# Kernel optimization log

Hardware: AMD Instinct MI355X
Metric: run time of the kernel (lower is better)

Reference implementation:

```python
import jax, jax.numpy as jnp
import numpy as np

B, N, NFEAT = 8, 5000, 15
NUM_CLASSES_IN = 12          # len(elem_labels)
D_IN = NUM_CLASSES_IN + NFEAT - 1  # 26
D_DIST = 256
D_HID = 256
BIN_SIZE = 100
NBINS = N // BIN_SIZE        # 50
K = 16                       # num_neighbors
DIST_MULT = 0.1
MAX_HALF_BINS = 100          # max_num_bins // 2
NUM_ID_OUT, NUM_REG_OUT = 8, 4


def _pairwise_dist(A):
    # A: [nbins, bs, d] -> [nbins, bs, bs]
    na = jnp.sum(A * A, -1)
    d2 = na[..., :, None] - 2.0 * jnp.einsum('...nd,...md->...nm', A, A) + na[..., None, :]
    return jnp.sqrt(jnp.maximum(d2, 1e-6))


def _build_edges(points, rot):
    # points: [N, D_DIST]; LSH binning then per-bin kNN (exp(-dist_mult * dist) affinities)
    mul = points @ rot[:, :NBINS // 2]
    cmul = jnp.concatenate([mul, -mul], axis=-1)
    bin_idx = jnp.argmax(cmul, axis=-1)
    bins_split = jnp.argsort(bin_idx).reshape(NBINS, BIN_SIZE)   # [nbins, bs] point ids
    parts = points[bins_split]                                   # [nbins, bs, d]
    dm = jnp.exp(-DIST_MULT * _pairwise_dist(parts))             # [nbins, bs, bs]
    vals, idx = jax.lax.top_k(dm, K)                             # [nbins, bs, K]
    dst = jax.vmap(lambda b, i: b[i])(bins_split, idx)           # global dst ids
    src = jnp.broadcast_to(bins_split[:, :, None], dst.shape)
    return src.reshape(-1), dst.reshape(-1), vals.reshape(-1)    # nnz = N*K


def _ghconv(x, src, dst, vals, theta, W_h, W_t, b_t):
    # x: [N, H]; edge list (src, dst, vals); duplicates sum, matching tf.sparse.add
    deg = jax.ops.segment_sum(vals, src, num_segments=N)
    norm = jnp.power(deg + 1e-6, -0.5)[:, None]
    f_hom = (x @ theta) * norm
    agg = jax.ops.segment_sum(vals[:, None] * f_hom[dst], src, num_segments=N) * norm
    f_het = x @ W_h
    gate = jax.nn.sigmoid(x @ W_t + b_t)
    return jax.nn.selu(gate * agg + (1.0 - gate) * f_het)


def setup_inputs() -> dict:
    key = jax.random.key(0)
    ks = jax.random.split(key, 32)
    w = lambda i, shape, s=0.02: (s * jax.random.normal(ks[i], shape)).astype(jnp.float32)
    ids = jax.random.randint(ks[0], (B, N, 1), 0, NUM_CLASSES_IN).astype(jnp.float32)
    props = jax.random.normal(ks[1], (B, N, NFEAT - 1), dtype=jnp.float32)
    X = jnp.concatenate([ids, props], axis=-1)
    return {
        'X': X,
        'rot': w(2, (D_DIST, MAX_HALF_BINS), 1.0),
        'W_emb': w(3, (D_IN, D_DIST)), 'b_emb': w(4, (D_DIST,)),
        'Wenc_id': w(5, (D_IN, D_HID)), 'benc_id': w(6, (D_HID,)),
        'theta_id': w(7, (D_HID, D_HID)), 'Wh_id': w(8, (D_HID, D_HID)),
        'Wt_id': w(9, (D_HID, D_HID)), 'bt_id': w(10, (D_HID,)),
        'Wdec_id': w(11, (D_HID, D_HID)), 'bdec_id': w(12, (D_HID,)),
        'Wout_id': w(13, (D_HID, NUM_ID_OUT)), 'bout_id': w(14, (NUM_ID_OUT,)),
        'Wenc_reg': w(15, (D_IN, D_HID)), 'benc_reg': w(16, (D_HID,)),
        'theta_reg': w(17, (D_HID, D_HID)), 'Wh_reg': w(18, (D_HID, D_HID)),
        'Wt_reg': w(19, (D_HID, D_HID)), 'bt_reg': w(20, (D_HID,)),
        'Wdec_reg': w(21, (D_HID, D_HID)), 'bdec_reg': w(22, (D_HID,)),
        'Wout_reg': w(23, (D_HID, NUM_REG_OUT)), 'bout_reg': w(24, (NUM_REG_OUT,)),
    }


def reference(X, rot, W_emb, b_emb,
              Wenc_id, benc_id, theta_id, Wh_id, Wt_id, bt_id, Wdec_id, bdec_id, Wout_id, bout_id,
              Wenc_reg, benc_reg, theta_reg, Wh_reg, Wt_reg, bt_reg, Wdec_reg, bdec_reg, Wout_reg, bout_reg):
    # InputEncoding: one-hot class id + remaining features
    enc = jnp.concatenate(
        [jax.nn.one_hot(X[:, :, 0].astype(jnp.int32), NUM_CLASSES_IN, dtype=jnp.float32),
         X[:, :, 1:]], axis=-1)                                  # [B, N, 26]
    emb = enc @ W_emb + b_emb                                     # distance embedding
    src, dst, vals = jax.vmap(_build_edges, in_axes=(0, None))(emb, rot)

    def branch(Wenc, benc, theta, Wh, Wt, bt, Wdec, bdec, Wout, bout):
        x = jax.nn.selu(enc @ Wenc + benc)
        x = jax.vmap(lambda xb, s, d, v: _ghconv(xb, s, d, v, theta, Wh, Wt, bt))(x, src, dst, vals)
        x = jax.nn.selu(x @ Wdec + bdec)
        return x @ Wout + bout

    out_id = branch(Wenc_id, benc_id, theta_id, Wh_id, Wt_id, bt_id, Wdec_id, bdec_id, Wout_id, bout_id)
    out_reg = branch(Wenc_reg, benc_reg, theta_reg, Wh_reg, Wt_reg, bt_reg, Wdec_reg, bdec_reg, Wout_reg, bout_reg)
    return out_id, out_reg
```

## Files before the change

### kernel.cpp

```cpp
#include <hip/hip_runtime.h>
#include <hip/hip_bf16.h>
#include <cstdint>
#include <cstddef>

#define NB     8
#define NLOC   5000
#define NPTS   40000
#define DIN    26
#define DH     256
#define NBINS  50
#define BSZ    100
#define KNN    16
#define KP     104

static const size_t OFF_BHI  = 40960000;
static const size_t OFF_BLO  = 41353216;
static const size_t OFF_BDHI = 41746432;
static const size_t OFF_BDLO = 41877504;
static const size_t OFF_ENC  = 81920000;
static const size_t OFF_BIN  = 86080000;
static const size_t OFF_ORD  = 86240000;
static const size_t OFF_NRM  = 86400000;
static const size_t OFF_EVAL = 86560000;
static const size_t OFF_EDST = 89120000;
static const size_t OFF_KEYS = 91680000;
static const size_t OFF_AXHI = 91680000;
static const size_t OFF_AXLO = 112160000;
static const size_t OFF_NA   = 132640000;
static const size_t OFF_FHET = 132640000;
static const size_t OFF_GATE = 173600000;

typedef __attribute__((ext_vector_type(8))) short short8;
typedef __attribute__((ext_vector_type(4))) float f32x4;

__device__ __forceinline__ float selu_f(float x) {
  const float scale = 1.0507009873554805f, alpha = 1.6732632423543772f;
  return x > 0.f ? scale * x : scale * alpha * expm1f(x);
}

__device__ __forceinline__ void split_bf16(float v, __hip_bfloat16& h, __hip_bfloat16& l) {
  h = __float2bfloat16(v);
  l = __float2bfloat16(v - __bfloat162float(h));
}

#define EPB 16
__global__ __launch_bounds__(256) void k_enc_emb(
    const float* __restrict__ X, const float* __restrict__ Wemb,
    const float* __restrict__ bemb, float* __restrict__ enc,
    double* __restrict__ emb) {
  __shared__ float xb[EPB * 15];
  const int tid = threadIdx.x;
  const int r0 = blockIdx.x * EPB;
  if (tid < EPB * 15) xb[tid] = X[(size_t)r0 * 15 + tid];
  double wcol[DIN];
  #pragma unroll
  for (int c = 0; c < DIN; c++) wcol[c] = (double)Wemb[c * DH + tid];
  const double bcol = (double)bemb[tid];
  __syncthreads();
  #pragma unroll 1
  for (int p = 0; p < EPB; p++) {
    const int id = (int)xb[p * 15];
    double acc = 0.0;
    #pragma unroll
    for (int c = 0; c < 12; c++)
      acc += ((c == id) ? 1.0 : 0.0) * wcol[c];
    #pragma unroll
    for (int c = 12; c < DIN; c++)
      acc += (double)xb[p * 15 + (c - 11)] * wcol[c];
    emb[(size_t)(r0 + p) * DH + tid] = acc + bcol;
  }
  #pragma unroll
  for (int t = 0; t < 2; t++) {
    int idx = t * 256 + tid;
    if (idx < EPB * DIN) {
      int p = idx / DIN, c = idx - p * DIN;
      int id = (int)xb[p * 15];
      float v = (c < 12) ? ((c == id) ? 1.f : 0.f) : xb[p * 15 + (c - 11)];
      enc[(size_t)(r0 + p) * DIN + c] = v;
    }
  }
}

#define MULPTS 16
__global__ __launch_bounds__(512) void k_mul(
    const double* __restrict__ emb, const float* __restrict__ rot,
    int* __restrict__ bin_idx) {
  __shared__ double ebuf[MULPTS][258];
  __shared__ float  rotT[25][257];
  __shared__ double mulb[MULPTS][26];
  const int tid = threadIdx.x;
  const int r0 = blockIdx.x * MULPTS;
  for (int idx = tid; idx < 25 * DH; idx += 512) {
    int d = idx / 25, j = idx - d * 25;
    rotT[j][d] = rot[d * 100 + j];
  }
  for (int idx = tid; idx < MULPTS * DH; idx += 512) {
    int p = idx >> 8, d = idx & 255;
    ebuf[p][d] = emb[(size_t)(r0 + p) * DH + d];
  }
  __syncthreads();
  if (tid < MULPTS * 25) {
    int p = tid / 25, j = tid - p * 25;
    double a = 0.0;
    #pragma unroll 4
    for (int d = 0; d < DH; d++) a += ebuf[p][d] * (double)rotT[j][d];
    mulb[p][j] = a;
  }
  __syncthreads();
  if (tid < MULPTS) {
    double best = -1e300; int bi = 0;
    #pragma unroll 1
    for (int jj = 0; jj < 2 * 25; jj++) {
      double v = (jj < 25) ? mulb[tid][jj] : -mulb[tid][jj - 25];
      if (v > best) { best = v; bi = jj; }
    }
    bin_idx[r0 + tid] = bi;
  }
}

#define SCH 20
__global__ __launch_bounds__(256) void k_sort(
    const int* __restrict__ bin_idx, int* __restrict__ order) {
  const int b = blockIdx.x;
  __shared__ unsigned short cnt[256][NBINS + 2];
  __shared__ int base[NBINS];
  __shared__ int bl[NLOC];
  const int tid = threadIdx.x;
  for (int j = 0; j < NBINS; j++) cnt[tid][j] = 0;
  for (int n = tid; n < NLOC; n += 256) bl[n] = bin_idx[b * NLOC + n];
  __syncthreads();
  const int s = tid * SCH;
  const int e = (s + SCH < NLOC) ? s + SCH : NLOC;
  for (int n = s; n < e; n++) cnt[tid][bl[n]]++;
  __syncthreads();
  if (tid < NBINS) {
    int run = 0;
    for (int t = 0; t < 256; t++) {
      int c = cnt[t][tid];
      cnt[t][tid] = (unsigned short)run;
      run += c;
    }
    base[tid] = run;
  }
  __syncthreads();
  if (tid == 0) {
    int r = 0;
    for (int j = 0; j < NBINS; j++) { int t = base[j]; base[j] = r; r += t; }
  }
  __syncthreads();
  for (int n = s; n < e; n++) {
    int j = bl[n];
    int pos = base[j] + cnt[tid][j];
    cnt[tid][j]++;
    order[b * NLOC + pos] = n;
  }
}

__global__ __launch_bounds__(256) void k_norm(
    const double* __restrict__ emb, const int* __restrict__ order,
    double* __restrict__ na) {
  const int s = blockIdx.x * 4 + (threadIdx.x >> 6);
  const int lane = threadIdx.x & 63;
  const int row = (s / NLOC) * NLOC + order[s];
  const double* p = &emb[(size_t)row * DH + lane * 4];
  double2 a = *(const double2*)p;
  double2 b = *(const double2*)(p + 2);
  double sum = a.x * a.x + a.y * a.y + b.x * b.x + b.y * b.y;
  #pragma unroll
  for (int off = 32; off >= 1; off >>= 1) sum += __shfl_xor(sum, off);
  if (lane == 0) na[s] = sum;
}

#define DQR 112
__global__ __launch_bounds__(256) void k_dist(
    const double* __restrict__ emb, const int* __restrict__ order,
    const double* __restrict__ na, double* __restrict__ keys) {
  __shared__ double P[DQR][34];
  __shared__ double naL[DQR];
  __shared__ int rid[DQR];
  const int bin = blockIdx.x;
  const int rh  = blockIdx.y;
  const int gb0 = bin * BSZ;
  const int brow = (bin / NBINS) * NLOC;
  const int tid = threadIdx.x;
  const int tx = tid & 15, ty = tid >> 4;
  if (tid < DQR) {
    int rr = tid < BSZ ? tid : BSZ - 1;
    rid[tid] = brow + order[gb0 + rr];
    naL[tid] = na[gb0 + rr];
  }
  __syncthreads();
  size_t srow[7];
  int scol[7], sr[7];
  #pragma unroll
  for (int q = 0; q < 7; q++) {
    int idx = q * 256 + tid;
    sr[q] = idx >> 4;
    scol[q] = (idx & 15) * 2;
    srow[q] = (size_t)rid[sr[q]] * DH;
  }
  int ar[4];
  #pragma unroll
  for (int i = 0; i < 4; i++) {
    int pr = rh * 50 + ty + 16 * i;
    ar[i] = pr < DQR ? pr : DQR - 1;
  }
  double acc[4][7] = {};
  double2 buf[7];
  #pragma unroll
  for (int q = 0; q < 7; q++)
    buf[q] = *(const double2*)&emb[srow[q] + scol[q]];
  for (int kc = 0; kc < 8; kc++) {
    __syncthreads();
    #pragma unroll
    for (int q = 0; q < 7; q++) {
      P[sr[q]][scol[q]]     = buf[q].x;
      P[sr[q]][scol[q] + 1] = buf[q].y;
    }
    __syncthreads();
    if (kc < 7) {
      #pragma unroll
      for (int q = 0; q < 7; q++)
        buf[q] = *(const double2*)&emb[srow[q] + (kc + 1) * 32 + scol[q]];
    }
    #pragma unroll 2
    for (int kk = 0; kk < 32; kk++) {
      double b[7];
      #pragma unroll
      for (int j = 0; j < 7; j++) b[j] = P[tx + 16 * j][kk];
      #pragma unroll
      for (int i = 0; i < 4; i++) {
        double a = P[ar[i]][kk];
        #pragma unroll
        for (int j = 0; j < 7; j++) acc[i][j] += a * b[j];
      }
    }
  }
  #pragma unroll
  for (int i = 0; i < 4; i++) {
    int lr = ty + 16 * i;
    if (lr >= 50) continue;
    int gi = rh * 50 + lr;
    #pragma unroll
    for (int j = 0; j < 7; j++) {
      int gj = tx + 16 * j;
      if (gj >= BSZ) continue;
      double t = naL[gi] - 2.0 * acc[i][j];
      t += naL[gj];
      keys[(size_t)(gb0 + gi) * KP + gj] = (t > 1e-6) ? t : 1e-6;
    }
  }
}

__global__ __launch_bounds__(256) void k_topk(
    const double* __restrict__ keys, float* __restrict__ evals,
    int* __restrict__ edstl, float* __restrict__ normv) {
  const int g = threadIdx.x >> 4;
  const int l = threadIdx.x & 15;
  const int row = blockIdx.x * 16 + g;
  const unsigned long long* kr =
      (const unsigned long long*)(keys + (size_t)row * KP);
  unsigned long long c[7];
  #pragma unroll
  for (int s = 0; s < 7; s++) {
    int j = s * 16 + l;
    c[s] = (j < BSZ) ? kr[j] : ~0ull;
  }
  float deg = 0.f, myev = 0.f;
  int myidx = 0;
  #pragma unroll 1
  for (int k = 0; k < KNN; k++) {
    unsigned long long mv = c[0];
    int ms = 0;
    #pragma unroll
    for (int s = 1; s < 7; s++)
      if (c[s] < mv) { mv = c[s]; ms = s; }
    int idx = ms * 16 + l;
    #pragma unroll
    for (int off = 8; off >= 1; off >>= 1) {
      unsigned long long ov = __shfl_xor(mv, off);
      int oi = __shfl_xor(idx, off);
      if (ov < mv || (ov == mv && oi < idx)) { mv = ov; idx = oi; }
    }
    float ev = expf(-0.1f * sqrtf((float)__longlong_as_double(mv)));
    deg += ev;
    if (l == k) { myev = ev; myidx = idx; }
    const int own = idx & 15, slot = idx >> 4;
    if (l == own) {
      #pragma unroll
      for (int s = 0; s < 7; s++)
        if (slot == s) c[s] = ~0ull;
    }
  }
  evals[(size_t)row * KNN + l] = myev;
  edstl[(size_t)row * KNN + l] = myidx;
  if (l == 0) normv[row] = 1.f / sqrtf(deg + 1e-6f);
}

__global__ __launch_bounds__(256) void k_encmm(
    const float* __restrict__ enc, const float* __restrict__ W,
    const float* __restrict__ bias, __hip_bfloat16* __restrict__ hi,
    __hip_bfloat16* __restrict__ lo) {
  const int r = blockIdx.x;
  __shared__ float e[DIN];
  const int tid = threadIdx.x;
  if (tid < DIN) e[tid] = enc[(size_t)r * DIN + tid];
  __syncthreads();
  float acc = 0.f;
  #pragma unroll 1
  for (int c = 0; c < DIN; c++) acc += e[c] * W[c * DH + tid];
  float v = selu_f(acc + bias[tid]);
  __hip_bfloat16 h, l;
  split_bf16(v, h, l);
  hi[(size_t)r * DH + tid] = h;
  lo[(size_t)r * DH + tid] = l;
}

__global__ __launch_bounds__(256) void k_cvt_w4(
    const float* __restrict__ W0, const float* __restrict__ W1,
    const float* __restrict__ W2, const float* __restrict__ W3,
    __hip_bfloat16* __restrict__ Bhi, __hip_bfloat16* __restrict__ Blo,
    __hip_bfloat16* __restrict__ Bdhi, __hip_bfloat16* __restrict__ Bdlo) {
  __shared__ float t[32][33];
  const int z = blockIdx.z;
  const float* W = (z == 0) ? W0 : (z == 1) ? W1 : (z == 2) ? W2 : W3;
  __hip_bfloat16* hi = (z < 3) ? Bhi + (size_t)z * 65536 : Bdhi;
  __hip_bfloat16* lo = (z < 3) ? Blo + (size_t)z * 65536 : Bdlo;
  const int tid = threadIdx.x, tx = tid & 31, ty = tid >> 5;
  const int k0 = blockIdx.x * 32, n0 = blockIdx.y * 32;
  #pragma unroll
  for (int r = 0; r < 4; r++)
    t[ty + r * 8][tx] = W[(size_t)(k0 + ty + r * 8) * 256 + n0 + tx];
  __syncthreads();
  #pragma unroll
  for (int r = 0; r < 4; r++) {
    int n = ty + r * 8;
    float v = t[tx][n];
    __hip_bfloat16 h, l;
    split_bf16(v, h, l);
    hi[(size_t)(n0 + n) * 256 + k0 + tx] = h;
    lo[(size_t)(n0 + n) * 256 + k0 + tx] = l;
  }
}

#define MF_SMEM (4 * 128 * 40 * 2)
template <int MODE>
__global__ __launch_bounds__(256, 4) void k_mfma(
    const ushort* __restrict__ Ahi, const ushort* __restrict__ Alo,
    const ushort* __restrict__ Bhi, const ushort* __restrict__ Blo,
    const float* __restrict__ bias,
    float* __restrict__ O0, float* __restrict__ O1, float* __restrict__ O2) {
  extern __shared__ char mfs[];
  short* As0 = (short*)mfs;
  short* As1 = As0 + 128 * 40;
  short* Bs0 = As1 + 128 * 40;
  short* Bs1 = Bs0 + 128 * 40;
  const int tid = threadIdx.x;
  const int m0 = blockIdx.y * 128;
  const int n0 = blockIdx.x * 128;
  const int lane = tid & 63, wid = tid >> 6;
  const int wr = wid >> 1, wc = wid & 1;
  const int lm = lane & 15, lg = lane >> 4;
  f32x4 acc[4][4];
  #pragma unroll
  for (int i = 0; i < 4; i++)
    #pragma unroll
    for (int j = 0; j < 4; j++)
      #pragma unroll
      for (int r = 0; r < 4; r++) acc[i][j][r] = 0.f;

  for (int k0 = 0; k0 < 256; k0 += 32) {
    #pragma unroll
    for (int it = 0; it < 2; it++) {
      int idx = it * 256 + tid;
      int r = idx >> 2, c = (idx & 3) * 8;
      int gm = m0 + r; if (gm >= NPTS) gm = NPTS - 1;
      *(uint4*)&As0[r * 40 + c] = *(const uint4*)&Ahi[(size_t)gm * 256 + k0 + c];
      *(uint4*)&As1[r * 40 + c] = *(const uint4*)&Alo[(size_t)gm * 256 + k0 + c];
      *(uint4*)&Bs0[r * 40 + c] = *(const uint4*)&Bhi[(size_t)(n0 + r) * 256 + k0 + c];
      *(uint4*)&Bs1[r * 40 + c] = *(const uint4*)&Blo[(size_t)(n0 + r) * 256 + k0 + c];
    }
    __syncthreads();
    const int lk = lg * 8;
    short8 aH[4], bH[4], aL[4], bL[4];
    #pragma unroll
    for (int mf = 0; mf < 4; mf++)
      aH[mf] = *(const short8*)&As0[(wr * 64 + mf * 16 + lm) * 40 + lk];
    #pragma unroll
    for (int nf = 0; nf < 4; nf++)
      bH[nf] = *(const short8*)&Bs0[(wc * 64 + nf * 16 + lm) * 40 + lk];
    #pragma unroll
    for (int mf = 0; mf < 4; mf++)
      #pragma unroll
      for (int nf = 0; nf < 4; nf++)
        acc[mf][nf] = __builtin_amdgcn_mfma_f32_16x16x32_bf16(aH[mf], bH[nf], acc[mf][nf], 0, 0, 0);
    #pragma unroll
    for (int nf = 0; nf < 4; nf++)
      bL[nf] = *(const short8*)&Bs1[(wc * 64 + nf * 16 + lm) * 40 + lk];
    #pragma unroll
    for (int mf = 0; mf < 4; mf++)
      #pragma unroll
      for (int nf = 0; nf < 4; nf++)
        acc[mf][nf] = __builtin_amdgcn_mfma_f32_16x16x32_bf16(aH[mf], bL[nf], acc[mf][nf], 0, 0, 0);
    #pragma unroll
    for (int mf = 0; mf < 4; mf++)
      aL[mf] = *(const short8*)&As1[(wr * 64 + mf * 16 + lm) * 40 + lk];
    #pragma unroll
    for (int mf = 0; mf < 4; mf++)
      #pragma unroll
      for (int nf = 0; nf < 4; nf++)
        acc[mf][nf] = __builtin_amdgcn_mfma_f32_16x16x32_bf16(aL[mf], bH[nf], acc[mf][nf], 0, 0, 0);
    __syncthreads();
  }

  float* Out; int cb;
  if (MODE == 0) {
    const int seg = blockIdx.x >> 1;
    Out = (seg == 0) ? O0 : ((seg == 1) ? O1 : O2);
    cb = (blockIdx.x & 1) * 128;
  } else {
    Out = O0; cb = n0;
  }
  const bool do_gate = (MODE == 0) && (blockIdx.x >> 1) == 2;
  #pragma unroll
  for (int mf = 0; mf < 4; mf++) {
    const int gm0 = m0 + wr * 64 + mf * 16 + lg * 4;
    #pragma unroll
    for (int nf = 0; nf < 4; nf++) {
      const int gn = cb + wc * 64 + nf * 16 + lm;
      #pragma unroll
      for (int r = 0; r < 4; r++) {
        const int gm = gm0 + r;
        if (gm >= NPTS) continue;
        float c = acc[mf][nf][r];
        if (MODE == 1)      c = selu_f(c + bias[gn]);
        else if (do_gate)   c = 1.f / (1.f + expf(-(c + bias[gn])));
        Out[(size_t)gm * 256 + gn] = c;
      }
    }
  }
}

#define GAT_SMEM (100 * 256 * 4 + 1600 * 8 + 100 * 4 + 100 * 4)
__global__ __launch_bounds__(1024) void k_gatherb(
    const float* __restrict__ hth, const float* __restrict__ fhet,
    const float* __restrict__ gate, const float* __restrict__ evals,
    const int* __restrict__ edstl, const int* __restrict__ order,
    const float* __restrict__ normv, __hip_bfloat16* __restrict__ yhi,
    __hip_bfloat16* __restrict__ ylo) {
  extern __shared__ char gsm[];
  float*  hl  = (float*)gsm;
  float2* cwL = (float2*)(gsm + 102400);
  int*    idsL = (int*)(gsm + 102400 + 12800);
  float*  nvL  = (float*)(gsm + 102400 + 12800 + 400);
  const int bin = blockIdx.x;
  const int gb0 = bin * 100;
  const int brow = (bin / NBINS) * NLOC;
  const int tid = threadIdx.x;
  const int p = tid >> 8, d = tid & 255;
  if (tid < BSZ) {
    idsL[tid] = order[gb0 + tid];
    nvL[tid] = normv[gb0 + tid];
  }
  __syncthreads();
  for (int t = tid; t < BSZ * KNN; t += 1024) {
    int lj = edstl[(size_t)gb0 * KNN + t];
    cwL[t] = make_float2(evals[(size_t)gb0 * KNN + t] * nvL[lj],
                         __int_as_float(lj));
  }
  for (int idx = tid; idx < BSZ * DH; idx += 1024) {
    int i = idx >> 8, dd = idx & 255;
    hl[i * 256 + dd] = hth[(size_t)(brow + idsL[i]) * DH + dd];
  }
  __syncthreads();
  size_t srow_n = (size_t)(brow + idsL[p]) * DH;
  float g_n = gate[srow_n + d], fh_n = fhet[srow_n + d];
  #pragma unroll 1
  for (int ii = 0; ii < 25; ii++) {
    const int i = ii * 4 + p;
    const size_t srow = srow_n;
    const float g = g_n, fh = fh_n;
    if (ii < 24) {
      srow_n = (size_t)(brow + idsL[i + 4]) * DH;
      g_n = gate[srow_n + d];
      fh_n = fhet[srow_n + d];
    }
    float acc = 0.f;
    #pragma unroll
    for (int k = 0; k < KNN; k++) {
      float2 cw = cwL[i * KNN + k];
      acc += cw.x * hl[__float_as_int(cw.y) * 256 + d];
    }
    float v = selu_f(g * (nvL[i] * acc) + (1.f - g) * fh);
    __hip_bfloat16 h, l;
    split_bf16(v, h, l);
    yhi[srow + d] = h;
    ylo[srow + d] = l;
  }
}

template <int OW>
__global__ __launch_bounds__(256) void k_out(
    const float* __restrict__ Z, const float* __restrict__ W,
    const float* __restrict__ bias, float* __restrict__ out) {
  const int p0 = blockIdx.x * 32;
  __shared__ float zb[32][257];
  const int tid = threadIdx.x;
  for (int idx = tid; idx < 32 * DH; idx += 256) {
    int p = idx >> 8, d = idx & 255;
    zb[p][d] = Z[(size_t)(p0 + p) * DH + d];
  }
  __syncthreads();
  if (tid < 32 * OW) {
    int p = tid / OW, o = tid - (tid / OW) * OW;
    float acc = 0.f;
    #pragma unroll 4
    for (int d = 0; d < DH; d++) acc += zb[p][d] * W[d * OW + o];
    out[(size_t)(p0 + p) * OW + o] = acc + bias[o];
  }
}

extern "C" void kernel_launch(void* const* d_in, const int* in_sizes, int n_in,
                              void* d_out, int out_size, void* d_ws, size_t ws_size,
                              hipStream_t stream) {
  const float* X     = (const float*)d_in[0];
  const float* rot   = (const float*)d_in[1];
  const float* W_emb = (const float*)d_in[2];
  const float* b_emb = (const float*)d_in[3];
  const float* Wenc[2]  = {(const float*)d_in[4],  (const float*)d_in[14]};
  const float* benc[2]  = {(const float*)d_in[5],  (const float*)d_in[15]};
  const float* theta[2] = {(const float*)d_in[6],  (const float*)d_in[16]};
  const float* Wh[2]    = {(const float*)d_in[7],  (const float*)d_in[17]};
  const float* Wt[2]    = {(const float*)d_in[8],  (const float*)d_in[18]};
  const float* bt[2]    = {(const float*)d_in[9],  (const float*)d_in[19]};
  const float* Wdec[2]  = {(const float*)d_in[10], (const float*)d_in[20]};
  const float* bdec[2]  = {(const float*)d_in[11], (const float*)d_in[21]};
  const float* Wout[2]  = {(const float*)d_in[12], (const float*)d_in[22]};
  const float* bout[2]  = {(const float*)d_in[13], (const float*)d_in[23]};

  char* w = (char*)d_ws;
  double* emb   = (double*)(w + 0);
  float*  hth   = (float*)(w + 0);
  __hip_bfloat16* Bhi  = (__hip_bfloat16*)(w + OFF_BHI);
  __hip_bfloat16* Blo  = (__hip_bfloat16*)(w + OFF_BLO);
  __hip_bfloat16* Bdhi = (__hip_bfloat16*)(w + OFF_BDHI);
  __hip_bfloat16* Bdlo = (__hip_bfloat16*)(w + OFF_BDLO);
  float*  enc   = (float*)(w + OFF_ENC);
  int*    binid = (int*)(w + OFF_BIN);
  int*    order = (int*)(w + OFF_ORD);
  float*  normv = (float*)(w + OFF_NRM);
  float*  evals = (float*)(w + OFF_EVAL);
  int*    edstl = (int*)(w + OFF_EDST);
  double* keys  = (double*)(w + OFF_KEYS);
  double* na    = (double*)(w + OFF_NA);
  __hip_bfloat16* Axhi = (__hip_bfloat16*)(w + OFF_AXHI);
  __hip_bfloat16* Axlo = (__hip_bfloat16*)(w + OFF_AXLO);
  float*  fhet  = (float*)(w + OFF_FHET);
  float*  gate  = (float*)(w + OFF_GATE);
  float*  zbuf  = (float*)(w + OFF_GATE);
  float*  outp  = (float*)d_out;

  (void)hipFuncSetAttribute(reinterpret_cast<const void*>(k_gatherb),
                            hipFuncAttributeMaxDynamicSharedMemorySize, GAT_SMEM);
  (void)hipFuncSetAttribute(reinterpret_cast<const void*>(k_mfma<0>),
                            hipFuncAttributeMaxDynamicSharedMemorySize, MF_SMEM);
  (void)hipFuncSetAttribute(reinterpret_cast<const void*>(k_mfma<1>),
                            hipFuncAttributeMaxDynamicSharedMemorySize, MF_SMEM);

  k_enc_emb<<<NPTS / EPB, 256, 0, stream>>>(X, W_emb, b_emb, enc, emb);
  k_mul<<<NPTS / MULPTS, 512, 0, stream>>>(emb, rot, binid);
  k_sort<<<NB, 256, 0, stream>>>(binid, order);
  k_norm<<<NPTS / 4, 256, 0, stream>>>(emb, order, na);
  k_dist<<<dim3(NB * NBINS, 2), 256, 0, stream>>>(emb, order, na, keys);
  k_topk<<<NPTS / 16, 256, 0, stream>>>(keys, evals, edstl, normv);

  const dim3 gw(8, 8, 4);
  const dim3 gf(6, 313), gd(2, 313);
  for (int br = 0; br < 2; br++) {
    k_cvt_w4<<<gw, 256, 0, stream>>>(theta[br], Wh[br], Wt[br], Wdec[br],
                                     Bhi, Blo, Bdhi, Bdlo);
    k_encmm<<<NPTS, 256, 0, stream>>>(enc, Wenc[br], benc[br], Axhi, Axlo);
    k_mfma<0><<<gf, 256, MF_SMEM, stream>>>((const ushort*)Axhi, (const ushort*)Axlo,
                                            (const ushort*)Bhi, (const ushort*)Blo,
                                            bt[br], hth, fhet, gate);
    k_gatherb<<<NB * NBINS, 1024, GAT_SMEM, stream>>>(hth, fhet, gate, evals, edstl,
                                                      order, normv, Axhi, Axlo);
    k_mfma<1><<<gd, 256, MF_SMEM, stream>>>((const ushort*)Axhi, (const ushort*)Axlo,
                                            (const ushort*)Bdhi, (const ushort*)Bdlo,
                                            bdec[br], zbuf, nullptr, nullptr);
    if (br == 0) k_out<8><<<NPTS / 32, 256, 0, stream>>>(zbuf, Wout[0], bout[0], outp);
    else         k_out<4><<<NPTS / 32, 256, 0, stream>>>(zbuf, Wout[1], bout[1], outp + (size_t)NPTS * 8);
  }
}
```

Before: 813.1 us.

## Prefetch next K-tile into registers and remap MFMA blocks per XCD

The split-bf16 MFMA GEMM now uses a 1D grid. Block indices are remapped so that consecutive tiles sharing the same A rows land on the same XCD, which should improve L2 reuse across the 8 chiplets. The global loads for the next 32-wide K slice are issued into registers right after the LDS store barrier, so they overlap the MFMA work on the current slice. The trailing barrier moves to the top of the loop. This costs 8 extra uint4 registers per thread and may lower occupancy.

```diff
diff --git a/kernel.cpp b/kernel.cpp
--- a/kernel.cpp
+++ b/kernel.cpp
@@ -355,9 +355,15 @@
   short* As1 = As0 + 128 * 40;
   short* Bs0 = As1 + 128 * 40;
   short* Bs1 = Bs0 + 128 * 40;
-  const int tid = threadIdx.x;
-  const int m0 = blockIdx.y * 128;
-  const int n0 = blockIdx.x * 128;
+  const int NX = (MODE == 0) ? 6 : 2;
+  const int total = NX * 313;
+  const int q = total >> 3, rr8 = total & 7;
+  const int xcd = blockIdx.x & 7, pos = blockIdx.x >> 3;
+  const int lw = (xcd < rr8 ? xcd * (q + 1) : rr8 * (q + 1) + (xcd - rr8) * q) + pos;
+  const int m0 = (lw / NX) * 128;
+  const int nx = lw - (lw / NX) * NX;
+  const int n0 = nx * 128;
+  const int tid = threadIdx.x;
   const int lane = tid & 63, wid = tid >> 6;
   const int wr = wid >> 1, wc = wid & 1;
   const int lm = lane & 15, lg = lane >> 4;
@@ -369,18 +375,44 @@
       #pragma unroll
       for (int r = 0; r < 4; r++) acc[i][j][r] = 0.f;
 
+  int srw[2]; size_t ga[2], gb[2];
+  #pragma unroll
+  for (int it = 0; it < 2; it++) {
+    int idx = it * 256 + tid;
+    int r = idx >> 2, c = (idx & 3) * 8;
+    srw[it] = r * 40 + c;
+    int gm = m0 + r; if (gm >= NPTS) gm = NPTS - 1;
+    ga[it] = (size_t)gm * 256 + c;
+    gb[it] = (size_t)(n0 + r) * 256 + c;
+  }
+  uint4 pf[8];
+  #pragma unroll
+  for (int it = 0; it < 2; it++) {
+    pf[it * 4 + 0] = *(const uint4*)&Ahi[ga[it]];
+    pf[it * 4 + 1] = *(const uint4*)&Alo[ga[it]];
+    pf[it * 4 + 2] = *(const uint4*)&Bhi[gb[it]];
+    pf[it * 4 + 3] = *(const uint4*)&Blo[gb[it]];
+  }
+
   for (int k0 = 0; k0 < 256; k0 += 32) {
+    __syncthreads();
     #pragma unroll
     for (int it = 0; it < 2; it++) {
-      int idx = it * 256 + tid;
-      int r = idx >> 2, c = (idx & 3) * 8;
-      int gm = m0 + r; if (gm >= NPTS) gm = NPTS - 1;
-      *(uint4*)&As0[r * 40 + c] = *(const uint4*)&Ahi[(size_t)gm * 256 + k0 + c];
-      *(uint4*)&As1[r * 40 + c] = *(const uint4*)&Alo[(size_t)gm * 256 + k0 + c];
-      *(uint4*)&Bs0[r * 40 + c] = *(const uint4*)&Bhi[(size_t)(n0 + r) * 256 + k0 + c];
-      *(uint4*)&Bs1[r * 40 + c] = *(const uint4*)&Blo[(size_t)(n0 + r) * 256 + k0 + c];
+      *(uint4*)&As0[srw[it]] = pf[it * 4 + 0];
+      *(uint4*)&As1[srw[it]] = pf[it * 4 + 1];
+      *(uint4*)&Bs0[srw[it]] = pf[it * 4 + 2];
+      *(uint4*)&Bs1[srw[it]] = pf[it * 4 + 3];
     }
     __syncthreads();
+    if (k0 < 224) {
+      #pragma unroll
+      for (int it = 0; it < 2; it++) {
+        pf[it * 4 + 0] = *(const uint4*)&Ahi[ga[it] + k0 + 32];
+        pf[it * 4 + 1] = *(const uint4*)&Alo[ga[it] + k0 + 32];
+        pf[it * 4 + 2] = *(const uint4*)&Bhi[gb[it] + k0 + 32];
+        pf[it * 4 + 3] = *(const uint4*)&Blo[gb[it] + k0 + 32];
+      }
+    }
     const int lk = lg * 8;
     short8 aH[4], bH[4], aL[4], bL[4];
     #pragma unroll
@@ -410,18 +442,17 @@
       #pragma unroll
       for (int nf = 0; nf < 4; nf++)
         acc[mf][nf] = __builtin_amdgcn_mfma_f32_16x16x32_bf16(aL[mf], bH[nf], acc[mf][nf], 0, 0, 0);
-    __syncthreads();
   }
 
   float* Out; int cb;
   if (MODE == 0) {
-    const int seg = blockIdx.x >> 1;
+    const int seg = nx >> 1;
     Out = (seg == 0) ? O0 : ((seg == 1) ? O1 : O2);
-    cb = (blockIdx.x & 1) * 128;
+    cb = (nx & 1) * 128;
   } else {
     Out = O0; cb = n0;
   }
-  const bool do_gate = (MODE == 0) && (blockIdx.x >> 1) == 2;
+  const bool do_gate = (MODE == 0) && (nx >> 1) == 2;
   #pragma unroll
   for (int mf = 0; mf < 4; mf++) {
     const int gm0 = m0 + wr * 64 + mf * 16 + lg * 4;
@@ -575,19 +606,18 @@
   k_topk<<<NPTS / 16, 256, 0, stream>>>(keys, evals, edstl, normv);
 
   const dim3 gw(8, 8, 4);
-  const dim3 gf(6, 313), gd(2, 313);
   for (int br = 0; br < 2; br++) {
     k_cvt_w4<<<gw, 256, 0, stream>>>(theta[br], Wh[br], Wt[br], Wdec[br],
                                      Bhi, Blo, Bdhi, Bdlo);
     k_encmm<<<NPTS, 256, 0, stream>>>(enc, Wenc[br], benc[br], Axhi, Axlo);
-    k_mfma<0><<<gf, 256, MF_SMEM, stream>>>((const ushort*)Axhi, (const ushort*)Axlo,
-                                            (const ushort*)Bhi, (const ushort*)Blo,
-                                            bt[br], hth, fhet, gate);
+    k_mfma<0><<<6 * 313, 256, MF_SMEM, stream>>>((const ushort*)Axhi, (const ushort*)Axlo,
+                                                 (const ushort*)Bhi, (const ushort*)Blo,
+                                                 bt[br], hth, fhet, gate);
     k_gatherb<<<NB * NBINS, 1024, GAT_SMEM, stream>>>(hth, fhet, gate, evals, edstl,
                                                       order, normv, Axhi, Axlo);
-    k_mfma<1><<<gd, 256, MF_SMEM, stream>>>((const ushort*)Axhi, (const ushort*)Axlo,
-                                            (const ushort*)Bdhi, (const ushort*)Bdlo,
-                                            bdec[br], zbuf, nullptr, nullptr);
+    k_mfma<1><<<2 * 313, 256, MF_SMEM, stream>>>((const ushort*)Axhi, (const ushort*)Axlo,
+                                                 (const ushort*)Bdhi, (const ushort*)Bdlo,
+                                                 bdec[br], zbuf, nullptr, nullptr);
     if (br == 0) k_out<8><<<NPTS / 32, 256, 0, stream>>>(zbuf, Wout[0], bout[0], outp);
     else         k_out<4><<<NPTS / 32, 256, 0, stream>>>(zbuf, Wout[1], bout[1], outp + (size_t)NPTS * 8);
   }
```

New measurement: 1.128 ms. 1.39x slower.
